# Optimization experiments

Hardware: AMD Instinct MI355X
Metric: run time of the kernel (lower is better)

## Reference

```python
import jax, jax.numpy as jnp
import numpy as np

N_NODES = 500_000
N_EDGES = 32_000_000
D_COEF = 1.0  # 'd' init arg, constant


def setup_inputs() -> dict:
    key = jax.random.key(0)
    k1, k2, k3 = jax.random.split(key, 3)
    theta = jax.random.normal(k1, (N_NODES, 1), dtype=jnp.float32)
    src = jax.random.randint(k2, (N_EDGES,), 0, N_NODES, dtype=jnp.int32)
    dst = jax.random.randint(k3, (N_EDGES,), 0, N_NODES, dtype=jnp.int32)
    logc = jnp.asarray(np.log(1.5), dtype=jnp.float32)  # continuousTimeVicsek2D.logc
    u0 = jnp.asarray(0.3, dtype=jnp.float32)
    return {"theta": theta, "logc": logc, "u0": u0, "src": src, "dst": dst}


def reference(theta, logc, u0, src, dst):
    # calc_message: dtheta = theta[src] - theta[dst]; m = exp(logc)*sin(d*dtheta)
    dtheta = theta[src] - theta[dst]              # [E,1] edge gather
    msg = jnp.exp(logc) * jnp.sin(dtheta * D_COEF)  # [E,1]
    # aggregate_message: mean over each node's incoming mailbox (segment mean by dst)
    n = theta.shape[0]
    w_sum = jax.ops.segment_sum(msg, dst, num_segments=n)          # [N,1]
    cnt = jax.ops.segment_sum(jnp.ones((dst.shape[0], 1), msg.dtype), dst, num_segments=n)
    w = w_sum / jnp.maximum(cnt, 1.0)             # [N,1] torque (0 if no in-edges)
    # polarity2velocity: v = u0 * [cos(theta), sin(theta)]
    v = u0 * jnp.concatenate([jnp.cos(theta), jnp.sin(theta)], axis=-1)  # [N,2]
    # return torque and velocity concatenated: [N,3] = [w | v]
    return jnp.concatenate([w, v], axis=-1)
```

## Files before the change

### kernel.cpp

```cpp
#include <hip/hip_runtime.h>


#define NB 123
#define BSHIFT 12
#define NODES_PER_B 4096
#define CAPB 272000u
#define TPB 256
#define EPT 16
#define EPI (TPB * EPT)
#define K_SLICES 8
#define TPB_R 512
#define Q_MASK 0xFFFFFu
#define DL_SHIFT 20

__global__ __launch_bounds__(TPB) void scatter_kernel(
    const float* __restrict__ theta,
    const int* __restrict__ src,
    const int* __restrict__ dst,
    unsigned int* __restrict__ recs,
    unsigned int* __restrict__ cursors,
    int n_edges, int n_iters)
{
    __shared__ unsigned int hist[NB];
    __shared__ unsigned int rankc[NB];
    __shared__ unsigned int offs[NB];
    __shared__ unsigned int gbase[NB];
    __shared__ unsigned int wsum0;
    __shared__ unsigned int sbuf[EPI];
    __shared__ unsigned char sbkt[EPI];

    const int tid = threadIdx.x;

    for (int iter = blockIdx.x; iter < n_iters; iter += gridDim.x) {
        const int base = iter * EPI + tid * EPT;

        for (int j = tid; j < NB; j += TPB) { hist[j] = 0; rankc[j] = 0; }
        __syncthreads();

        unsigned int myrec[EPT];
        int myb[EPT];

        if (base + EPT <= n_edges) {
            int4 s4[4], d4[4];
            #pragma unroll
            for (int q = 0; q < 4; ++q) {
                s4[q] = ((const int4*)(src + base))[q];
                d4[q] = ((const int4*)(dst + base))[q];
            }
            const int* sp = (const int*)s4;
            const int* dp = (const int*)d4;
            float tg[EPT];
            #pragma unroll
            for (int j = 0; j < EPT; ++j) tg[j] = theta[sp[j]];
            #pragma unroll
            for (int j = 0; j < EPT; ++j) {
                int b = dp[j] >> BSHIFT;
                myb[j] = b;
                atomicAdd(&hist[b], 1u);
            }
            #pragma unroll
            for (int j = 0; j < EPT; ++j) {
                float tc = fminf(fmaxf(tg[j], -8.0f), 8.0f);
                unsigned int q = (unsigned int)fmaf(tc, 65536.0f, 524288.5f);
                if (q > Q_MASK) q = Q_MASK;
                myrec[j] = (((unsigned int)(dp[j] & (NODES_PER_B - 1))) << DL_SHIFT) | q;
            }
        } else {
            #pragma unroll
            for (int j = 0; j < EPT; ++j) {
                int e = base + j;
                if (e < n_edges) {
                    int dn = dst[e];
                    float tc = fminf(fmaxf(theta[src[e]], -8.0f), 8.0f);
                    unsigned int q = (unsigned int)fmaf(tc, 65536.0f, 524288.5f);
                    if (q > Q_MASK) q = Q_MASK;
                    myrec[j] = (((unsigned int)(dn & (NODES_PER_B - 1))) << DL_SHIFT) | q;
                    int b = dn >> BSHIFT;
                    myb[j] = b;
                    atomicAdd(&hist[b], 1u);
                } else {
                    myb[j] = -1;
                }
            }
        }
        __syncthreads();

        unsigned int h = 0, x = 0;
        if (tid < 128) {
            h = (tid < NB) ? hist[tid] : 0u;
            x = h;
            #pragma unroll
            for (int dlt = 1; dlt < 64; dlt <<= 1) {
                unsigned int y = __shfl_up(x, dlt, 64);
                if ((tid & 63) >= dlt) x += y;
            }
            if (tid == 63) wsum0 = x;
        }
        __syncthreads();
        if (tid < 128) {
            if (tid >= 64) x += wsum0;
            if (tid < NB) {
                offs[tid] = x - h;
                gbase[tid] = h ? atomicAdd(&cursors[tid], h) : 0u;
            }
        }
        __syncthreads();

        #pragma unroll
        for (int j = 0; j < EPT; ++j) {
            int b = myb[j];
            if (b >= 0) {
                unsigned int r = atomicAdd(&rankc[b], 1u);
                unsigned int slot = offs[b] + r;
                sbuf[slot] = myrec[j];
                sbkt[slot] = (unsigned char)b;
            }
        }
        __syncthreads();

        unsigned int total = offs[NB - 1] + hist[NB - 1];
        for (unsigned int slot = tid; slot < total; slot += TPB) {
            unsigned int b = sbkt[slot];
            unsigned int gpos = gbase[b] + (slot - offs[b]);
            if (gpos < CAPB) recs[(size_t)b * CAPB + gpos] = sbuf[slot];
        }
        __syncthreads();
    }
}

__device__ __forceinline__ void proc_rec(unsigned int ru, unsigned long long* acc)
{
    float t = fmaf((float)(ru & Q_MASK), 1.0f / 65536.0f, -8.0f);
    float s, co;
    __sincosf(t, &s, &co);
    unsigned int ps = (unsigned int)fmaf(s, 8192.0f, 16384.5f);
    unsigned int pc = (unsigned int)fmaf(co, 8192.0f, 16384.5f);
    atomicAdd(&acc[ru >> DL_SHIFT],
              ((unsigned long long)ps << 37) | ((unsigned long long)pc << 10) | 1ull);
}

__global__ __launch_bounds__(TPB_R, 8) void reduce_kernel(
    const unsigned int* __restrict__ recs,
    const unsigned int* __restrict__ cursors,
    unsigned long long* __restrict__ acc_g)
{
    __shared__ unsigned long long acc[NODES_PER_B];
    const int tid = threadIdx.x;
    const int b = blockIdx.x >> 3;
    const int k = blockIdx.x & 7;

    for (int j = tid; j < NODES_PER_B; j += TPB_R) acc[j] = 0ull;
    __syncthreads();

    unsigned int cnt = cursors[b];
    if (cnt > CAPB) cnt = CAPB;
    unsigned int slice = (((cnt + K_SLICES - 1) / K_SLICES) + 15u) & ~15u;
    unsigned int lo = (unsigned int)k * slice;
    if (lo > cnt) lo = cnt;
    unsigned int hi = lo + slice; if (hi > cnt) hi = cnt;

    const unsigned int* bp = recs + (size_t)b * CAPB;

    const unsigned int chunk = TPB_R * 4u;
    unsigned int nfull = (hi > lo) ? (hi - lo) / chunk : 0u;
    unsigned int vend = lo + nfull * chunk;

    for (unsigned int b2 = lo; b2 < vend; b2 += chunk) {
        uint4 r = *(const uint4*)(bp + b2 + (unsigned int)tid * 4u);
        proc_rec(r.x, acc);
        proc_rec(r.y, acc);
        proc_rec(r.z, acc);
        proc_rec(r.w, acc);
    }
    for (unsigned int j = vend + tid; j < hi; j += TPB_R) proc_rec(bp[j], acc);
    __syncthreads();

    unsigned long long* ag = acc_g + (size_t)b * NODES_PER_B;
    for (int j = tid; j < NODES_PER_B; j += TPB_R) {
        unsigned long long v = acc[j];
        if (v) atomicAdd(&ag[j], v);
    }
}

__global__ __launch_bounds__(TPB) void node_kernel(
    const float* __restrict__ theta,
    const float* __restrict__ logc,
    const float* __restrict__ u0p,
    const unsigned long long* __restrict__ acc_g,
    float* __restrict__ out,
    int n_nodes)
{
    int i = blockIdx.x * TPB + threadIdx.x;
    if (i >= n_nodes) return;

    unsigned long long a = acc_g[i];
    int cnt = (int)(a & 1023ull);
    int pcS = (int)((a >> 10) & 0x7FFFFFFull);
    int psS = (int)(a >> 37);
    float sinS = (float)(psS - cnt * 16384) * (1.0f / 8192.0f);
    float cosS = (float)(pcS - cnt * 16384) * (1.0f / 8192.0f);

    float t = theta[i];
    float sd, cd;
    __sincosf(t, &sd, &cd);
    float c = __expf(logc[0]);
    float w = c * (cd * sinS - sd * cosS) / fmaxf((float)cnt, 1.0f);
    float u0 = u0p[0];
    out[3 * i + 0] = w;
    out[3 * i + 1] = u0 * cd;
    out[3 * i + 2] = u0 * sd;
}

__global__ __launch_bounds__(256) void edge_kernel_fb(
    const float* __restrict__ theta, const float* __restrict__ logc,
    const int* __restrict__ src, const int* __restrict__ dst,
    unsigned long long* __restrict__ acc, int n_edges)
{
    const float c = __expf(logc[0]);
    int base = (blockIdx.x * 256 + threadIdx.x) * 4;
    if (base + 3 < n_edges) {
        int4 s4 = *(const int4*)(src + base);
        int4 d4 = *(const int4*)(dst + base);
        float m0 = c * __sinf(theta[s4.x] - theta[d4.x]);
        float m1 = c * __sinf(theta[s4.y] - theta[d4.y]);
        float m2 = c * __sinf(theta[s4.z] - theta[d4.z]);
        float m3 = c * __sinf(theta[s4.w] - theta[d4.w]);
        atomicAdd(&acc[d4.x], ((unsigned long long)((m0 + 2.0f) * 1073741824.0f) << 24) | 1ull);
        atomicAdd(&acc[d4.y], ((unsigned long long)((m1 + 2.0f) * 1073741824.0f) << 24) | 1ull);
        atomicAdd(&acc[d4.z], ((unsigned long long)((m2 + 2.0f) * 1073741824.0f) << 24) | 1ull);
        atomicAdd(&acc[d4.w], ((unsigned long long)((m3 + 2.0f) * 1073741824.0f) << 24) | 1ull);
    } else {
        for (int e = base; e < n_edges; ++e) {
            int s = src[e], d = dst[e];
            float m = c * __sinf(theta[s] - theta[d]);
            atomicAdd(&acc[d], ((unsigned long long)((m + 2.0f) * 1073741824.0f) << 24) | 1ull);
        }
    }
}

__global__ __launch_bounds__(256) void node_kernel_fb(
    const float* __restrict__ theta, const float* __restrict__ u0p,
    const unsigned long long* __restrict__ acc, float* __restrict__ out, int n_nodes)
{
    int i = blockIdx.x * 256 + threadIdx.x;
    if (i >= n_nodes) return;
    unsigned long long p = acc[i];
    long long cnt = (long long)(p & 0xFFFFFFull);
    long long net = (long long)(p >> 24) - (cnt << 31);
    float sum = (float)((double)net * (1.0 / 1073741824.0));
    float w = sum / fmaxf((float)cnt, 1.0f);
    float t = theta[i]; float u0 = u0p[0];
    out[3 * i + 0] = w;
    out[3 * i + 1] = u0 * __cosf(t);
    out[3 * i + 2] = u0 * __sinf(t);
}

extern "C" void kernel_launch(void* const* d_in, const int* in_sizes, int n_in,
                              void* d_out, int out_size, void* d_ws, size_t ws_size,
                              hipStream_t stream) {
    const float* theta = (const float*)d_in[0];
    const float* logc  = (const float*)d_in[1];
    const float* u0    = (const float*)d_in[2];
    const int*   src   = (const int*)d_in[3];
    const int*   dst   = (const int*)d_in[4];
    float* out = (float*)d_out;

    int n_nodes = in_sizes[0];
    int n_edges = in_sizes[3];

    size_t recs_bytes  = (size_t)NB * CAPB * sizeof(unsigned int);
    size_t cursors_off = (recs_bytes + 255) & ~(size_t)255;
    size_t acc_off     = cursors_off + 512;
    size_t acc_bytes   = (size_t)NB * NODES_PER_B * sizeof(unsigned long long);
    size_t need = acc_off + acc_bytes;

    bool fast = (ws_size >= need) && (n_nodes <= NB * NODES_PER_B);

    if (fast) {
        unsigned int* recs          = (unsigned int*)d_ws;
        unsigned int* cursors       = (unsigned int*)((char*)d_ws + cursors_off);
        unsigned long long* acc_g   = (unsigned long long*)((char*)d_ws + acc_off);

        hipMemsetAsync(cursors, 0, 512 + acc_bytes, stream);

        int n_iters = (n_edges + EPI - 1) / EPI;
        scatter_kernel<<<n_iters, TPB, 0, stream>>>(theta, src, dst, recs,
                                                    cursors, n_edges, n_iters);

        reduce_kernel<<<NB * K_SLICES, TPB_R, 0, stream>>>(recs, cursors, acc_g);

        int nblocks = (n_nodes + TPB - 1) / TPB;
        node_kernel<<<nblocks, TPB, 0, stream>>>(theta, logc, u0, acc_g, out, n_nodes);
    } else {
        unsigned long long* acc = (unsigned long long*)d_ws;
        hipMemsetAsync(d_ws, 0, (size_t)n_nodes * sizeof(unsigned long long), stream);
        int eblocks = (n_edges + 1023) / 1024;
        edge_kernel_fb<<<eblocks, 256, 0, stream>>>(theta, logc, src, dst, acc, n_edges);
        int nblocks = (n_nodes + 255) / 256;
        node_kernel_fb<<<nblocks, 255 + 1, 0, stream>>>(theta, u0, acc, out, n_nodes);
    }
}
```

Before: 456.4 us.

## Split edge binning into two passes: bucket by src, then gather theta from LDS

Edges are first bucketed by source-node block without reading theta. A second pass loads each source block's theta into shared memory, looks up theta[src] locally, quantizes it, and re-buckets the records by destination block for the existing reduce kernel. This replaces random global gathers of theta[src] with LDS lookups. In exchange it adds a full extra write and read of the 32M-entry record array plus a second workspace buffer, and only runs if the workspace is large enough.

New measurement: 564.3 us. 1.24x slower.

```diff
diff --git a/kernel.cpp b/kernel.cpp
--- a/kernel.cpp
+++ b/kernel.cpp
@@ -8,12 +8,239 @@
 #define TPB 256
 #define EPT 16
 #define EPI (TPB * EPT)
+#define CHUNKS2 67
 #define K_SLICES 8
 #define TPB_R 512
 #define Q_MASK 0xFFFFFu
 #define DL_SHIFT 20
-
-__global__ __launch_bounds__(TPB) void scatter_kernel(
+#define DST_MASK 0x7FFFFu
+
+
+__global__ __launch_bounds__(TPB) void scatter1_kernel(
+    const int* __restrict__ src,
+    const int* __restrict__ dst,
+    unsigned int* __restrict__ recs1,
+    unsigned int* __restrict__ cursors1,
+    int n_edges, int n_iters)
+{
+    __shared__ unsigned int hist[NB];
+    __shared__ unsigned int rankc[NB];
+    __shared__ unsigned int offs[NB];
+    __shared__ unsigned int gbase[NB];
+    __shared__ unsigned int wsum0;
+    __shared__ unsigned int sbuf[EPI];
+    __shared__ unsigned char sbkt[EPI];
+
+    const int tid = threadIdx.x;
+
+    for (int iter = blockIdx.x; iter < n_iters; iter += gridDim.x) {
+        const int base = iter * EPI + tid * EPT;
+
+        for (int j = tid; j < NB; j += TPB) { hist[j] = 0; rankc[j] = 0; }
+        __syncthreads();
+
+        unsigned int myrec[EPT];
+        int myb[EPT];
+
+        if (base + EPT <= n_edges) {
+            int4 s4[4], d4[4];
+            #pragma unroll
+            for (int q = 0; q < 4; ++q) {
+                s4[q] = ((const int4*)(src + base))[q];
+                d4[q] = ((const int4*)(dst + base))[q];
+            }
+            const int* sp = (const int*)s4;
+            const int* dp = (const int*)d4;
+            #pragma unroll
+            for (int j = 0; j < EPT; ++j) {
+                int sn = sp[j];
+                int b = sn >> BSHIFT;
+                myb[j] = b;
+                myrec[j] = (((unsigned int)(sn & (NODES_PER_B - 1))) << 19)
+                         | (unsigned int)dp[j];
+                atomicAdd(&hist[b], 1u);
+            }
+        } else {
+            #pragma unroll
+            for (int j = 0; j < EPT; ++j) {
+                int e = base + j;
+                if (e < n_edges) {
+                    int sn = src[e];
+                    int b = sn >> BSHIFT;
+                    myb[j] = b;
+                    myrec[j] = (((unsigned int)(sn & (NODES_PER_B - 1))) << 19)
+                             | (unsigned int)dst[e];
+                    atomicAdd(&hist[b], 1u);
+                } else {
+                    myb[j] = -1;
+                }
+            }
+        }
+        __syncthreads();
+
+        unsigned int h = 0, x = 0;
+        if (tid < 128) {
+            h = (tid < NB) ? hist[tid] : 0u;
+            x = h;
+            #pragma unroll
+            for (int dlt = 1; dlt < 64; dlt <<= 1) {
+                unsigned int y = __shfl_up(x, dlt, 64);
+                if ((tid & 63) >= dlt) x += y;
+            }
+            if (tid == 63) wsum0 = x;
+        }
+        __syncthreads();
+        if (tid < 128) {
+            if (tid >= 64) x += wsum0;
+            if (tid < NB) {
+                offs[tid] = x - h;
+                gbase[tid] = h ? atomicAdd(&cursors1[tid], h) : 0u;
+            }
+        }
+        __syncthreads();
+
+        #pragma unroll
+        for (int j = 0; j < EPT; ++j) {
+            int b = myb[j];
+            if (b >= 0) {
+                unsigned int r = atomicAdd(&rankc[b], 1u);
+                unsigned int slot = offs[b] + r;
+                sbuf[slot] = myrec[j];
+                sbkt[slot] = (unsigned char)b;
+            }
+        }
+        __syncthreads();
+
+        unsigned int total = offs[NB - 1] + hist[NB - 1];
+        for (unsigned int slot = tid; slot < total; slot += TPB) {
+            unsigned int b = sbkt[slot];
+            unsigned int gpos = gbase[b] + (slot - offs[b]);
+            if (gpos < CAPB) recs1[(size_t)b * CAPB + gpos] = sbuf[slot];
+        }
+        __syncthreads();
+    }
+}
+
+__global__ __launch_bounds__(TPB) void scatter2_kernel(
+    const float* __restrict__ theta,
+    const unsigned int* __restrict__ recs1,
+    const unsigned int* __restrict__ cursors1,
+    unsigned int* __restrict__ recs2,
+    unsigned int* __restrict__ cursors2,
+    int n_nodes)
+{
+    const int sb = blockIdx.y;
+    unsigned int cnt = cursors1[sb];
+    if (cnt > CAPB) cnt = CAPB;
+    unsigned int lo = (unsigned int)blockIdx.x * EPI;
+    if (lo >= cnt) return;
+    unsigned int hi = lo + EPI; if (hi > cnt) hi = cnt;
+
+    __shared__ float thd[NODES_PER_B];
+    __shared__ unsigned int hist[NB];
+    __shared__ unsigned int rankc[NB];
+    __shared__ unsigned int offs[NB];
+    __shared__ unsigned int gbase[NB];
+    __shared__ unsigned int wsum0;
+    __shared__ unsigned int sbuf[EPI];
+    __shared__ unsigned char sbkt[EPI];
+
+    const int tid = threadIdx.x;
+    const int nbase = sb * NODES_PER_B;
+
+    for (int j = tid; j < NODES_PER_B; j += TPB) {
+        int g = nbase + j;
+        thd[j] = (g < n_nodes) ? theta[g] : 0.0f;
+    }
+    for (int j = tid; j < NB; j += TPB) { hist[j] = 0; rankc[j] = 0; }
+    __syncthreads();
+
+    const unsigned int* bp = recs1 + (size_t)sb * CAPB;
+    const unsigned int rb = lo + (unsigned int)tid * EPT;
+
+    unsigned int myrec[EPT];
+    int myb[EPT];
+
+    if (rb + EPT <= hi) {
+        uint4 r4[4];
+        #pragma unroll
+        for (int q = 0; q < 4; ++q) r4[q] = ((const uint4*)(bp + rb))[q];
+        const unsigned int* rp = (const unsigned int*)r4;
+        #pragma unroll
+        for (int j = 0; j < EPT; ++j) {
+            unsigned int r = rp[j];
+            unsigned int dn = r & DST_MASK;
+            int b = (int)(dn >> BSHIFT);
+            myb[j] = b;
+            float tc = fminf(fmaxf(thd[r >> 19], -8.0f), 8.0f);
+            unsigned int q = (unsigned int)fmaf(tc, 65536.0f, 524288.5f);
+            if (q > Q_MASK) q = Q_MASK;
+            myrec[j] = ((dn & (NODES_PER_B - 1)) << DL_SHIFT) | q;
+            atomicAdd(&hist[b], 1u);
+        }
+    } else {
+        #pragma unroll
+        for (int j = 0; j < EPT; ++j) {
+            unsigned int e = rb + j;
+            if (e < hi) {
+                unsigned int r = bp[e];
+                unsigned int dn = r & DST_MASK;
+                int b = (int)(dn >> BSHIFT);
+                myb[j] = b;
+                float tc = fminf(fmaxf(thd[r >> 19], -8.0f), 8.0f);
+                unsigned int q = (unsigned int)fmaf(tc, 65536.0f, 524288.5f);
+                if (q > Q_MASK) q = Q_MASK;
+                myrec[j] = ((dn & (NODES_PER_B - 1)) << DL_SHIFT) | q;
+                atomicAdd(&hist[b], 1u);
+            } else {
+                myb[j] = -1;
+            }
+        }
+    }
+    __syncthreads();
+
+    unsigned int h = 0, x = 0;
+    if (tid < 128) {
+        h = (tid < NB) ? hist[tid] : 0u;
+        x = h;
+        #pragma unroll
+        for (int dlt = 1; dlt < 64; dlt <<= 1) {
+            unsigned int y = __shfl_up(x, dlt, 64);
+            if ((tid & 63) >= dlt) x += y;
+        }
+        if (tid == 63) wsum0 = x;
+    }
+    __syncthreads();
+    if (tid < 128) {
+        if (tid >= 64) x += wsum0;
+        if (tid < NB) {
+            offs[tid] = x - h;
+            gbase[tid] = h ? atomicAdd(&cursors2[tid], h) : 0u;
+        }
+    }
+    __syncthreads();
+
+    #pragma unroll
+    for (int j = 0; j < EPT; ++j) {
+        int b = myb[j];
+        if (b >= 0) {
+            unsigned int r = atomicAdd(&rankc[b], 1u);
+            unsigned int slot = offs[b] + r;
+            sbuf[slot] = myrec[j];
+            sbkt[slot] = (unsigned char)b;
+        }
+    }
+    __syncthreads();
+
+    unsigned int total = offs[NB - 1] + hist[NB - 1];
+    for (unsigned int slot = tid; slot < total; slot += TPB) {
+        unsigned int b = sbkt[slot];
+        unsigned int gpos = gbase[b] + (slot - offs[b]);
+        if (gpos < CAPB) recs2[(size_t)b * CAPB + gpos] = sbuf[slot];
+    }
+}
+
+__global__ __launch_bounds__(TPB) void scatter_mid_kernel(
     const float* __restrict__ theta,
     const int* __restrict__ src,
     const int* __restrict__ dst,
@@ -268,24 +495,51 @@
     int n_nodes = in_sizes[0];
     int n_edges = in_sizes[3];
 
-    size_t recs_bytes  = (size_t)NB * CAPB * sizeof(unsigned int);
-    size_t cursors_off = (recs_bytes + 255) & ~(size_t)255;
-    size_t acc_off     = cursors_off + 512;
-    size_t acc_bytes   = (size_t)NB * NODES_PER_B * sizeof(unsigned long long);
-    size_t need = acc_off + acc_bytes;
-
-    bool fast = (ws_size >= need) && (n_nodes <= NB * NODES_PER_B);
-
-    if (fast) {
-        unsigned int* recs          = (unsigned int*)d_ws;
-        unsigned int* cursors       = (unsigned int*)((char*)d_ws + cursors_off);
-        unsigned long long* acc_g   = (unsigned long long*)((char*)d_ws + acc_off);
-
-        hipMemsetAsync(cursors, 0, 512 + acc_bytes, stream);
+    size_t recs_bytes = (size_t)NB * CAPB * sizeof(unsigned int);
+    size_t acc_bytes  = (size_t)NB * NODES_PER_B * sizeof(unsigned long long);
+
+    size_t f_recs2_off   = recs_bytes;
+    size_t f_cur_off     = (f_recs2_off + recs_bytes + 255) & ~(size_t)255;
+    size_t f_acc_off     = f_cur_off + 1024;
+    size_t need_full     = f_acc_off + acc_bytes;
+
+    size_t m_cur_off = (recs_bytes + 255) & ~(size_t)255;
+    size_t m_acc_off = m_cur_off + 512;
+    size_t need_mid  = m_acc_off + acc_bytes;
+
+    bool nodes_ok = (n_nodes <= NB * NODES_PER_B);
+
+    if (ws_size >= need_full && nodes_ok) {
+        unsigned int* recs1    = (unsigned int*)d_ws;
+        unsigned int* recs2    = (unsigned int*)((char*)d_ws + f_recs2_off);
+        unsigned int* cursors1 = (unsigned int*)((char*)d_ws + f_cur_off);
+        unsigned int* cursors2 = cursors1 + 128;
+        unsigned long long* acc_g = (unsigned long long*)((char*)d_ws + f_acc_off);
+
+        (void)hipMemsetAsync(cursors1, 0, 1024 + acc_bytes, stream);
 
         int n_iters = (n_edges + EPI - 1) / EPI;
-        scatter_kernel<<<n_iters, TPB, 0, stream>>>(theta, src, dst, recs,
-                                                    cursors, n_edges, n_iters);
+        scatter1_kernel<<<n_iters, TPB, 0, stream>>>(src, dst, recs1, cursors1,
+                                                     n_edges, n_iters);
+
+        dim3 g2(CHUNKS2, NB);
+        scatter2_kernel<<<g2, TPB, 0, stream>>>(theta, recs1, cursors1,
+                                                recs2, cursors2, n_nodes);
+
+        reduce_kernel<<<NB * K_SLICES, TPB_R, 0, stream>>>(recs2, cursors2, acc_g);
+
+        int nblocks = (n_nodes + TPB - 1) / TPB;
+        node_kernel<<<nblocks, TPB, 0, stream>>>(theta, logc, u0, acc_g, out, n_nodes);
+    } else if (ws_size >= need_mid && nodes_ok) {
+        unsigned int* recs     = (unsigned int*)d_ws;
+        unsigned int* cursors  = (unsigned int*)((char*)d_ws + m_cur_off);
+        unsigned long long* acc_g = (unsigned long long*)((char*)d_ws + m_acc_off);
+
+        (void)hipMemsetAsync(cursors, 0, 512 + acc_bytes, stream);
+
+        int n_iters = (n_edges + EPI - 1) / EPI;
+        scatter_mid_kernel<<<n_iters, TPB, 0, stream>>>(theta, src, dst, recs,
+                                                        cursors, n_edges, n_iters);
 
         reduce_kernel<<<NB * K_SLICES, TPB_R, 0, stream>>>(recs, cursors, acc_g);
 
@@ -293,10 +547,10 @@
         node_kernel<<<nblocks, TPB, 0, stream>>>(theta, logc, u0, acc_g, out, n_nodes);
     } else {
         unsigned long long* acc = (unsigned long long*)d_ws;
-        hipMemsetAsync(d_ws, 0, (size_t)n_nodes * sizeof(unsigned long long), stream);
+        (void)hipMemsetAsync(d_ws, 0, (size_t)n_nodes * sizeof(unsigned long long), stream);
         int eblocks = (n_edges + 1023) / 1024;
         edge_kernel_fb<<<eblocks, 256, 0, stream>>>(theta, logc, src, dst, acc, n_edges);
         int nblocks = (n_nodes + 255) / 256;
-        node_kernel_fb<<<nblocks, 255 + 1, 0, stream>>>(theta, u0, acc, out, n_nodes);
-    }
-}
+        node_kernel_fb<<<nblocks, 256, 0, stream>>>(theta, u0, acc, out, n_nodes);
+    }
+}
```
